# Kernel tuning notes

Hardware: AMD Instinct MI355X
Metric: run time of the kernel (lower is better)

Reference implementation:

```python
import jax, jax.numpy as jnp
import numpy as np

N_NODES = 50000
N_EDGES = 1000000
D_IN = 128
HID = 64
N_GRAPHS = 256
NEG_SLOPE = 0.2


def _gatv2_layer(x, src, dst, Wl, Wr, att, b, n_nodes):
    # lin_l applied to source nodes, lin_r to target nodes (PyG GATv2Conv, heads=1)
    xl = x @ Wl.T  # [N, C]
    xr = x @ Wr.T  # [N, C]
    e = jax.nn.leaky_relu(xl[src] + xr[dst], NEG_SLOPE)  # [E, C]
    logits = e @ att  # [E]
    # segment softmax over destination node
    m = jax.ops.segment_max(logits, dst, num_segments=n_nodes)
    ex = jnp.exp(logits - m[dst])
    den = jax.ops.segment_sum(ex, dst, num_segments=n_nodes)
    alpha = ex / den[dst]  # [E]
    out = jax.ops.segment_sum(alpha[:, None] * xl[src], dst, num_segments=n_nodes)
    return out + b


def setup_inputs() -> dict:
    key = jax.random.key(0)
    ks = jax.random.split(key, 32)
    x = jax.random.normal(ks[0], (N_NODES, D_IN), dtype=jnp.float32)
    edge_index = jax.random.randint(ks[1], (2, N_EDGES), 0, N_NODES, dtype=jnp.int64)
    batch = jnp.sort(jax.random.randint(ks[2], (N_NODES,), 0, N_GRAPHS, dtype=jnp.int64))
    inp = {"x": x, "edge_index": edge_index, "batch": batch}
    dims = [D_IN, HID, HID]  # input dim per layer
    kidx = 3
    for i, din in enumerate(dims):
        inp[f"Wl{i}"] = jax.random.normal(ks[kidx], (HID, din), dtype=jnp.float32) * 0.1; kidx += 1
        inp[f"Wr{i}"] = jax.random.normal(ks[kidx], (HID, din), dtype=jnp.float32) * 0.1; kidx += 1
        inp[f"att{i}"] = jax.random.normal(ks[kidx], (HID,), dtype=jnp.float32) * 0.1; kidx += 1
        inp[f"b{i}"] = jnp.zeros((HID,), dtype=jnp.float32)
        inp[f"Rw{i}"] = jax.random.normal(ks[kidx], (HID, din), dtype=jnp.float32) * 0.1; kidx += 1
        inp[f"Rb{i}"] = jnp.zeros((HID,), dtype=jnp.float32)
    inp["Wf"] = jax.random.normal(ks[kidx], (1, HID), dtype=jnp.float32) * 0.1
    inp["bf"] = jnp.zeros((1,), dtype=jnp.float32)
    return inp


def reference(x, edge_index, batch, Wl0, Wr0, att0, b0, Rw0, Rb0,
              Wl1, Wr1, att1, b1, Rw1, Rb1,
              Wl2, Wr2, att2, b2, Rw2, Rb2, Wf, bf):
    n = x.shape[0]
    # add_self_loops=True (PyG default)
    loops = jnp.arange(n, dtype=edge_index.dtype)
    src = jnp.concatenate([edge_index[0], loops])
    dst = jnp.concatenate([edge_index[1], loops])
    layers = [(Wl0, Wr0, att0, b0, Rw0, Rb0),
              (Wl1, Wr1, att1, b1, Rw1, Rb1),
              (Wl2, Wr2, att2, b2, Rw2, Rb2)]
    for i, (Wl, Wr, att, b, Rw, Rb) in enumerate(layers):
        h = _gatv2_layer(x, src, dst, Wl, Wr, att, b, n) + (x @ Rw.T + Rb)  # res=True
        # norm=None -> Identity; dropout inactive at inference
        x = jax.nn.relu(h) if i < len(layers) - 1 else h
    # global_mean_pool
    sums = jax.ops.segment_sum(x, batch, num_segments=N_GRAPHS)
    cnt = jax.ops.segment_sum(jnp.ones((n,), x.dtype), batch, num_segments=N_GRAPHS)
    pooled = sums / jnp.maximum(cnt, 1.0)[:, None]
    return pooled @ Wf.T + bf
```

## Files before the change

### kernel.cpp

```cpp
#include <hip/hip_runtime.h>


#define NN 50000
#define NE 1000000
#define HID 64
#define DIN0 128
#define NG 256
#define NEG 0.2f

#define SCHUNK 1024
#define SNB ((NN + SCHUNK - 1) / SCHUNK)

typedef float f32x4 __attribute__((ext_vector_type(4)));
typedef short s8v __attribute__((ext_vector_type(8)));
typedef short s4v __attribute__((ext_vector_type(4)));
typedef __bf16 bf16x8 __attribute__((ext_vector_type(8)));
typedef _Float16 h2v __attribute__((ext_vector_type(2)));
typedef unsigned short u16;

__device__ __forceinline__ unsigned short f2bf(float f) {
    unsigned u = __float_as_uint(f);
    u = u + 0x7fffu + ((u >> 16) & 1u);
    return (unsigned short)(u >> 16);
}
__device__ __forceinline__ float bf2f(unsigned short v) {
    return __uint_as_float(((unsigned)v) << 16);
}
__device__ __forceinline__ short split_hi(float x) {
    return (short)f2bf(x);
}
__device__ __forceinline__ short split_lo(float x, short hi) {
    return (short)f2bf(x - bf2f((unsigned short)hi));
}
__device__ __forceinline__ h2v u2h(unsigned u) { return __builtin_bit_cast(h2v, u); }
__device__ __forceinline__ unsigned h2u(h2v h) { return __builtin_bit_cast(unsigned, h); }
__device__ __forceinline__ float hx(unsigned u, int hi) {
    h2v h = __builtin_bit_cast(h2v, u);
    return (float)h[hi];
}

__global__ __launch_bounds__(256) void k_wt_all(
        const float* __restrict__ Wl0, const float* __restrict__ Wr0, const float* __restrict__ Rw0,
        const float* __restrict__ Wl1, const float* __restrict__ Wr1, const float* __restrict__ Rw1,
        const float* __restrict__ Wl2, const float* __restrict__ Wr2, const float* __restrict__ Rw2,
        short* __restrict__ Ws0, short* __restrict__ Ws1, short* __restrict__ Ws2,
        int* __restrict__ startg, int* __restrict__ endg) {
    int i = blockIdx.x * 256 + threadIdx.x;
    if (i < 2 * NG) {
        if (i < NG) startg[i] = 0; else endg[i - NG] = 0;
    }
    const int L0N = 3 * HID * DIN0;
    const int L1N = 3 * HID * HID;
    if (i >= L0N + 2 * L1N) return;
    const float* Wm; short* Ws; int din, local;
    if (i < L0N) {
        local = i; din = DIN0; Ws = Ws0;
        int m = local / (DIN0 * HID);
        Wm = (m == 0) ? Wl0 : (m == 1) ? Wr0 : Rw0;
    } else if (i < L0N + L1N) {
        local = i - L0N; din = HID; Ws = Ws1;
        int m = local / (HID * HID);
        Wm = (m == 0) ? Wl1 : (m == 1) ? Wr1 : Rw1;
    } else {
        local = i - L0N - L1N; din = HID; Ws = Ws2;
        int m = local / (HID * HID);
        Wm = (m == 0) ? Wl2 : (m == 1) ? Wr2 : Rw2;
    }
    int m = local / (din * HID);
    int r = local - m * (din * HID);
    int c = r / din, k = r - c * din;
    float w = Wm[c * din + k];
    short hi = split_hi(w);
    short lo = split_lo(w, hi);
    Ws[(((m * 2 + 0) * HID + c) * din) + k] = hi;
    Ws[(((m * 2 + 1) * HID + c) * din) + k] = lo;
}

__global__ void k_bounds(const int* __restrict__ batch,
                         int* __restrict__ startg, int* __restrict__ endg,
                         int* __restrict__ cnt8) {
    int i = blockIdx.x * 256 + threadIdx.x;
    if (i >= NN) return;
#pragma unroll
    for (int g = 0; g < 8; g++) cnt8[g * NN + i] = 0;
    int g = batch[i];
    if (i == 0 || batch[i - 1] != g) startg[g] = i;
    if (i == NN - 1 || batch[i + 1] != g) endg[g] = i + 1;
}

__global__ __launch_bounds__(256) void k_hist8(const int* __restrict__ edst,
                                               int* __restrict__ cnt8,
                                               u16* __restrict__ rank) {
    int* mycnt = cnt8 + (blockIdx.x & 7) * NN;
    for (int e = blockIdx.x * 256 + threadIdx.x; e < NE; e += 512 * 256) {
        int r = atomicAdd(&mycnt[edst[e]], 1);
        rank[e] = (u16)r;
    }
}

__global__ void k_hist_red(int* __restrict__ cnt8, int* __restrict__ cnt) {
    int i = blockIdx.x * 256 + threadIdx.x;
    if (i >= NN) return;
    int s = 1;
#pragma unroll
    for (int g = 0; g < 8; g++) {
        int t = cnt8[g * NN + i];
        cnt8[g * NN + i] = s;
        s += t;
    }
    cnt[i] = s;
}

__global__ __launch_bounds__(256) void k_scan_part(const int* __restrict__ cnt,
                                                   int* __restrict__ part) {
    __shared__ int ws[4];
    int b = blockIdx.x, t = threadIdx.x;
    int i0 = b * SCHUNK + t * 4;
    int s = 0;
#pragma unroll
    for (int j = 0; j < 4; j++) {
        int i = i0 + j;
        if (i < NN) s += cnt[i];
    }
#pragma unroll
    for (int o = 32; o; o >>= 1) s += __shfl_xor(s, o, 64);
    if ((t & 63) == 0) ws[t >> 6] = s;
    __syncthreads();
    if (t == 0) part[b] = ws[0] + ws[1] + ws[2] + ws[3];
}

__global__ void k_scan_small(const int* __restrict__ part, int* __restrict__ partScan) {
    __shared__ int sh[SNB];
    int t = threadIdx.x;
    if (t < SNB) sh[t] = part[t];
    __syncthreads();
    if (t < SNB) {
        int s = 0;
        for (int i = 0; i < t; i++) s += sh[i];
        partScan[t] = s;
    }
}

__global__ __launch_bounds__(256) void k_scan_emit(const int* __restrict__ cnt,
                                                   const int* __restrict__ partScan,
                                                   int* __restrict__ off,
                                                   u16* __restrict__ srcs) {
    __shared__ int tsum[256];
    int b = blockIdx.x, t = threadIdx.x;
    int i0 = b * SCHUNK + t * 4;
    int e[4], p[4];
    int s = 0;
#pragma unroll
    for (int j = 0; j < 4; j++) {
        int i = i0 + j;
        e[j] = (i < NN) ? cnt[i] : 0;
        p[j] = s;
        s += e[j];
    }
    tsum[t] = s;
    __syncthreads();
    for (int d = 1; d < 256; d <<= 1) {
        int v = (t >= d) ? tsum[t - d] : 0;
        __syncthreads();
        tsum[t] += v;
        __syncthreads();
    }
    int base = partScan[b] + ((t == 0) ? 0 : tsum[t - 1]);
#pragma unroll
    for (int j = 0; j < 4; j++) {
        int i = i0 + j;
        if (i < NN) {
            int v = base + p[j];
            off[i] = v;
            srcs[v] = (u16)i;
            if (i == NN - 1) off[NN] = v + e[j];
        }
    }
}

__global__ __launch_bounds__(256) void k_scatter_rank(
        const int* __restrict__ esrc, const int* __restrict__ edst,
        const int* __restrict__ off, const int* __restrict__ cnt8,
        const u16* __restrict__ rank, u16* __restrict__ srcs) {
    int e = blockIdx.x * 256 + threadIdx.x;
    if (e >= NE) return;
    int d = edst[e];
    int slice = (e >> 8) & 7;
    int pos = off[d] + cnt8[slice * NN + d] + (int)rank[e];
    srcs[pos] = (u16)esrc[e];
}

template <int DIN, bool RELU>
__global__ __launch_bounds__(256, 3) void k_gemm(
        const float* __restrict__ xin, const short* __restrict__ Ws,
        const float* __restrict__ bvec, const float* __restrict__ rb,
        _Float16* __restrict__ xl16, float* __restrict__ xr, float* __restrict__ acc) {
    constexpr int LROW = 40;
    __shared__ short lds[20480];
    short* xhi = lds;
    short* xlo = lds + 2560;

    const int tid = threadIdx.x;
    const int w = tid >> 6;
    const int lane = tid & 63;
    const int col = lane & 15;
    const int quad = lane >> 4;
    const int nb0 = blockIdx.x * 64;

    f32x4 d[3][4];
#pragma unroll
    for (int m = 0; m < 3; m++)
#pragma unroll
        for (int ct = 0; ct < 4; ct++) d[m][ct] = (f32x4){0.f, 0.f, 0.f, 0.f};

    for (int c0 = 0; c0 < DIN; c0 += 32) {
        if (c0) __syncthreads();
        for (int u = tid; u < 512; u += 256) {
            int row = u >> 3, kq = u & 7;
            int n = nb0 + row;
            float4 v = make_float4(0.f, 0.f, 0.f, 0.f);
            if (n < NN) {
                v = *(const float4*)&xin[(size_t)n * DIN + c0 + 4 * kq];
                if (RELU) {
                    v.x = fmaxf(v.x, 0.f); v.y = fmaxf(v.y, 0.f);
                    v.z = fmaxf(v.z, 0.f); v.w = fmaxf(v.w, 0.f);
                }
            }
            s4v h, l;
            short h0 = split_hi(v.x), l0 = split_lo(v.x, h0);
            short h1 = split_hi(v.y), l1 = split_lo(v.y, h1);
            short h2 = split_hi(v.z), l2 = split_lo(v.z, h2);
            short h3 = split_hi(v.w), l3 = split_lo(v.w, h3);
            h[0] = h0; h[1] = h1; h[2] = h2; h[3] = h3;
            l[0] = l0; l[1] = l1; l[2] = l2; l[3] = l3;
            *(s4v*)&xhi[row * LROW + 4 * kq] = h;
            *(s4v*)&xlo[row * LROW + 4 * kq] = l;
        }
        for (int u = tid; u < 1536; u += 256) {
            int mp = u >> 8;
            int r = u & 255;
            int c = r >> 2, q = r & 3;
            s8v v = *(const s8v*)&Ws[((mp * HID + c) * DIN) + c0 + 8 * q];
            *(s8v*)&lds[5120 + mp * 2560 + c * LROW + 8 * q] = v;
        }
        __syncthreads();

        bf16x8 a_h = __builtin_bit_cast(bf16x8,
            *(const s8v*)&xhi[(w * 16 + col) * LROW + quad * 8]);
        bf16x8 a_l = __builtin_bit_cast(bf16x8,
            *(const s8v*)&xlo[(w * 16 + col) * LROW + quad * 8]);

#pragma unroll
        for (int m = 0; m < 3; m++) {
#pragma unroll
            for (int ct = 0; ct < 4; ct++) {
                bf16x8 b_h = __builtin_bit_cast(bf16x8,
                    *(const s8v*)&lds[5120 + (m * 2 + 0) * 2560 + (ct * 16 + col) * LROW + quad * 8]);
                bf16x8 b_l = __builtin_bit_cast(bf16x8,
                    *(const s8v*)&lds[5120 + (m * 2 + 1) * 2560 + (ct * 16 + col) * LROW + quad * 8]);
                d[m][ct] = __builtin_amdgcn_mfma_f32_16x16x32_bf16(a_h, b_h, d[m][ct], 0, 0, 0);
                d[m][ct] = __builtin_amdgcn_mfma_f32_16x16x32_bf16(a_h, b_l, d[m][ct], 0, 0, 0);
                d[m][ct] = __builtin_amdgcn_mfma_f32_16x16x32_bf16(a_l, b_h, d[m][ct], 0, 0, 0);
            }
        }
    }

#pragma unroll
    for (int r = 0; r < 4; r++) {
        int n = nb0 + w * 16 + quad * 4 + r;
        if (n >= NN) continue;
        size_t base = (size_t)n * HID;
#pragma unroll
        for (int ct = 0; ct < 4; ct++) {
            int c = ct * 16 + col;
            xl16[base + c] = (_Float16)d[0][ct][r];
            xr[base + c] = d[1][ct][r];
            acc[base + c] = d[2][ct][r] + bvec[c] + rb[c];
        }
    }
}

__global__ __launch_bounds__(256) void k_attn_dst(
        const int* __restrict__ off, const u16* __restrict__ srcs,
        const _Float16* __restrict__ xl16, const float* __restrict__ xr,
        const float* __restrict__ att, float* __restrict__ acc) {
    const int lane = threadIdx.x & 63;
    const int d = blockIdx.x * 4 + (threadIdx.x >> 6);
    if (d >= NN) return;
    const int e = lane >> 3;
    const int cg = lane & 7;

    const float4* xr4 = (const float4*)&xr[(size_t)d * HID + 8 * cg];
    float4 xra = xr4[0], xrb = xr4[1];
    const float4* at4 = (const float4*)&att[8 * cg];
    float4 ata = at4[0], atb = at4[1];
    h2v xh0 = {(_Float16)xra.x, (_Float16)xra.y};
    h2v xh1 = {(_Float16)xra.z, (_Float16)xra.w};
    h2v xh2 = {(_Float16)xrb.x, (_Float16)xrb.y};
    h2v xh3 = {(_Float16)xrb.z, (_Float16)xrb.w};
    h2v a6h0 = {(_Float16)(0.6f * ata.x), (_Float16)(0.6f * ata.y)};
    h2v a6h1 = {(_Float16)(0.6f * ata.z), (_Float16)(0.6f * ata.w)};
    h2v a6h2 = {(_Float16)(0.6f * atb.x), (_Float16)(0.6f * atb.y)};
    h2v a6h3 = {(_Float16)(0.6f * atb.z), (_Float16)(0.6f * atb.w)};
    h2v a4h0 = {(_Float16)(0.4f * ata.x), (_Float16)(0.4f * ata.y)};
    h2v a4h1 = {(_Float16)(0.4f * ata.z), (_Float16)(0.4f * ata.w)};
    h2v a4h2 = {(_Float16)(0.4f * atb.x), (_Float16)(0.4f * atb.y)};
    h2v a4h3 = {(_Float16)(0.4f * atb.z), (_Float16)(0.4f * atb.w)};

#define EDGE_LOGIT(S, U, T)                                                    \
    {                                                                          \
        U = *(const uint4*)&xl16[(size_t)(S) * HID + 8 * cg];                  \
        h2v _v; unsigned _a; float _ps;                                        \
        _v = u2h(U.x) + xh0; _a = h2u(_v) & 0x7FFF7FFFu;                       \
        _ps = __builtin_amdgcn_fdot2(a6h0, _v, 0.f, false);                    \
        _ps = __builtin_amdgcn_fdot2(a4h0, u2h(_a), _ps, false);               \
        _v = u2h(U.y) + xh1; _a = h2u(_v) & 0x7FFF7FFFu;                       \
        _ps = __builtin_amdgcn_fdot2(a6h1, _v, _ps, false);                    \
        _ps = __builtin_amdgcn_fdot2(a4h1, u2h(_a), _ps, false);               \
        _v = u2h(U.z) + xh2; _a = h2u(_v) & 0x7FFF7FFFu;                       \
        _ps = __builtin_amdgcn_fdot2(a6h2, _v, _ps, false);                    \
        _ps = __builtin_amdgcn_fdot2(a4h2, u2h(_a), _ps, false);               \
        _v = u2h(U.w) + xh3; _a = h2u(_v) & 0x7FFF7FFFu;                       \
        _ps = __builtin_amdgcn_fdot2(a6h3, _v, _ps, false);                    \
        _ps = __builtin_amdgcn_fdot2(a4h3, u2h(_a), _ps, false);               \
        _ps += __shfl_xor(_ps, 1, 64);                                         \
        _ps += __shfl_xor(_ps, 2, 64);                                         \
        _ps += __shfl_xor(_ps, 4, 64);                                         \
        T = _ps;                                                               \
    }

#define ACC8(OP)                                                               \
    oA.x = OP(oA.x, hx(U0.x, 0), hx(U1.x, 0));                                 \
    oA.y = OP(oA.y, hx(U0.x, 1), hx(U1.x, 1));                                 \
    oA.z = OP(oA.z, hx(U0.y, 0), hx(U1.y, 0));                                 \
    oA.w = OP(oA.w, hx(U0.y, 1), hx(U1.y, 1));                                 \
    oB.x = OP(oB.x, hx(U0.z, 0), hx(U1.z, 0));                                 \
    oB.y = OP(oB.y, hx(U0.z, 1), hx(U1.z, 1));                                 \
    oB.z = OP(oB.z, hx(U0.w, 0), hx(U1.w, 0));                                 \
    oB.w = OP(oB.w, hx(U0.w, 1), hx(U1.w, 1));
#define OP_RS(o, x0, x1) fmaf(o, corr, fmaf(p0, x0, p1 * (x1)))
#define OP_NR(o, x0, x1) fmaf(p0, x0, fmaf(p1, (x1), o))

    float m = -INFINITY, l = 0.f;
    float4 oA = make_float4(0.f, 0.f, 0.f, 0.f);
    float4 oB = make_float4(0.f, 0.f, 0.f, 0.f);

    const int lo = off[d], deg = off[d + 1] - lo;
    int sv = 0;
    if (lane < 16) sv = (int)srcs[lo + min(lane, deg - 1)];
    for (int base = 0; base < deg; base += 16) {
        int svc = sv;
        if (base + 16 < deg && lane < 16)
            sv = (int)srcs[lo + min(base + 16 + lane, deg - 1)];
        int s0 = __shfl(svc, e, 64);
        int s1 = __shfl(svc, e + 8, 64);

        uint4 U0, U1; float t0, t1;
        EDGE_LOGIT(s0, U0, t0);
        EDGE_LOGIT(s1, U1, t1);
        if (base + e >= deg) t0 = -INFINITY;
        if (base + 8 + e >= deg) t1 = -INFINITY;

        float cm = fmaxf(t0, t1);
        cm = fmaxf(cm, __shfl_xor(cm, 8, 64));
        cm = fmaxf(cm, __shfl_xor(cm, 16, 64));
        cm = fmaxf(cm, __shfl_xor(cm, 32, 64));
        if (cm > m) {
            float corr = __expf(m - cm);
            float p0 = __expf(t0 - cm);
            float p1 = __expf(t1 - cm);
            m = cm;
            l = fmaf(l, corr, p0 + p1);
            ACC8(OP_RS)
        } else {
            float p0 = __expf(t0 - m);
            float p1 = __expf(t1 - m);
            l += p0 + p1;
            ACC8(OP_NR)
        }
    }
#undef EDGE_LOGIT
#undef ACC8
#undef OP_RS
#undef OP_NR

#pragma unroll
    for (int w = 8; w <= 32; w <<= 1) {
        l    += __shfl_xor(l, w, 64);
        oA.x += __shfl_xor(oA.x, w, 64); oA.y += __shfl_xor(oA.y, w, 64);
        oA.z += __shfl_xor(oA.z, w, 64); oA.w += __shfl_xor(oA.w, w, 64);
        oB.x += __shfl_xor(oB.x, w, 64); oB.y += __shfl_xor(oB.y, w, 64);
        oB.z += __shfl_xor(oB.z, w, 64); oB.w += __shfl_xor(oB.w, w, 64);
    }

    if (e == 0) {
        float inv = 1.f / l;
        float4* a4 = (float4*)&acc[(size_t)d * HID + 8 * cg];
        float4 c0 = a4[0], c1 = a4[1];
        c0.x += oA.x * inv; c0.y += oA.y * inv;
        c0.z += oA.z * inv; c0.w += oA.w * inv;
        c1.x += oB.x * inv; c1.y += oB.y * inv;
        c1.z += oB.z * inv; c1.w += oB.w * inv;
        a4[0] = c0; a4[1] = c1;
    }
}

__global__ __launch_bounds__(512) void k_pool_final(
        const float* __restrict__ acc,
        const int* __restrict__ startg, const int* __restrict__ endg,
        const float* __restrict__ Wf, const float* __restrict__ bf_,
        float* __restrict__ out) {
    __shared__ float red[8][HID];
    const int g = blockIdx.x;
    const int c = threadIdx.x & 63;
    const int j = threadIdx.x >> 6;
    const int s = startg[g], epos = endg[g];

    float sum = 0.f;
    for (int n = s + j; n < epos; n += 8)
        sum += acc[(size_t)n * HID + c];
    red[j][c] = sum;
    __syncthreads();

    if (threadIdx.x < HID) {
        float tot = 0.f;
#pragma unroll
        for (int w = 0; w < 8; w++) tot += red[w][c];
        float cntf = (float)(epos - s);
        float v = tot / fmaxf(cntf, 1.f) * Wf[c];
#pragma unroll
        for (int o = 32; o; o >>= 1) v += __shfl_xor(v, o, 64);
        if (c == 0) out[g] = v + bf_[0];
    }
}

extern "C" void kernel_launch(void* const* d_in, const int* in_sizes, int n_in,
                              void* d_out, int out_size, void* d_ws, size_t ws_size,
                              hipStream_t stream) {
    const float* x   = (const float*)d_in[0];
    const int* eidx  = (const int*)d_in[1];
    const int* batch = (const int*)d_in[2];
    const int* esrc = eidx;
    const int* edst = eidx + NE;
    const float* Wf  = (const float*)d_in[21];
    const float* bfb = (const float*)d_in[22];

    float* wsf = (float*)d_ws;
    const size_t NN64 = (size_t)NN * HID;
    _Float16* xl16 = (_Float16*)wsf;
    float* xr     = wsf + NN64;
    float* acc0   = xr + NN64;
    float* acc1   = acc0 + NN64;
    short* Ws0    = (short*)(acc1 + NN64);
    short* Ws1    = Ws0 + 2 * 3 * HID * DIN0;
    short* Ws2    = Ws1 + 2 * 3 * HID * HID;
    int*   ccnt   = (int*)(Ws2 + 2 * 3 * HID * HID);
    int*   startg = ccnt + NN;
    int*   endg   = startg + NG;
    int*   off    = endg + NG;
    int*   part   = off + NN + 1;
    int*   partSc = part + SNB;
    int*   cnt8   = partSc + SNB;
    u16*   rank   = (u16*)(cnt8 + 8 * NN);
    u16*   srcs   = rank + NE;

    k_wt_all<<<(3 * HID * DIN0 + 2 * 3 * HID * HID + 255) / 256, 256, 0, stream>>>(
        (const float*)d_in[3], (const float*)d_in[4], (const float*)d_in[7],
        (const float*)d_in[9], (const float*)d_in[10], (const float*)d_in[13],
        (const float*)d_in[15], (const float*)d_in[16], (const float*)d_in[19],
        Ws0, Ws1, Ws2, startg, endg);
    k_bounds<<<(NN + 255) / 256, 256, 0, stream>>>(batch, startg, endg, cnt8);

    k_hist8<<<512, 256, 0, stream>>>(edst, cnt8, rank);
    k_hist_red<<<(NN + 255) / 256, 256, 0, stream>>>(cnt8, ccnt);
    k_scan_part<<<SNB, 256, 0, stream>>>(ccnt, part);
    k_scan_small<<<1, 64, 0, stream>>>(part, partSc);
    k_scan_emit<<<SNB, 256, 0, stream>>>(ccnt, partSc, off, srcs);
    k_scatter_rank<<<(NE + 255) / 256, 256, 0, stream>>>(esrc, edst, off, cnt8, rank, srcs);

    const short* Wss[3] = {Ws0, Ws1, Ws2};
    float* accs[4] = {acc0, acc0, acc1, acc0};
    const int gemm_grid = (NN + 63) / 64;
    for (int L = 0; L < 3; L++) {
        const float* att = (const float*)d_in[3 + L * 6 + 2];
        const float* b   = (const float*)d_in[3 + L * 6 + 3];
        const float* Rb  = (const float*)d_in[3 + L * 6 + 5];
        float* accOut = accs[L + 1];

        if (L == 0)
            k_gemm<DIN0, false><<<gemm_grid, 256, 0, stream>>>(
                x, Wss[0], b, Rb, xl16, xr, accOut);
        else
            k_gemm<HID, true><<<gemm_grid, 256, 0, stream>>>(
                accs[L], Wss[L], b, Rb, xl16, xr, accOut);

        k_attn_dst<<<(NN + 3) / 4, 256, 0, stream>>>(off, srcs, xl16, xr, att, accOut);
    }

    k_pool_final<<<NG, 512, 0, stream>>>(accs[3], startg, endg, Wf, bfb, (float*)d_out);
}
```

Before: 358.1 us.

## Process 32 edges per attention iteration with fp16 dot aggregation and fp16 xr

The attention kernel now handles 32 edges per loop iteration (four per lane group) instead of 16, which exposes more independent gathers per wave. The weighted aggregation uses packed fp16 fdot2 with fp16 softmax weights in place of scalar fp32 FMAs, and the online-softmax rescale is split out of the accumulation. xr is stored as fp16 by the GEMM, and the scaled attention vectors are precomputed once in the weight-prep kernel, which cuts per-node conversion and load traffic. The cost is lower precision, since probabilities and xr are rounded to fp16, and higher register pressure from four in-flight edge vectors.

```diff
diff --git a/kernel.cpp b/kernel.cpp
--- a/kernel.cpp
+++ b/kernel.cpp
@@ -34,20 +34,31 @@
 }
 __device__ __forceinline__ h2v u2h(unsigned u) { return __builtin_bit_cast(h2v, u); }
 __device__ __forceinline__ unsigned h2u(h2v h) { return __builtin_bit_cast(unsigned, h); }
-__device__ __forceinline__ float hx(unsigned u, int hi) {
-    h2v h = __builtin_bit_cast(h2v, u);
-    return (float)h[hi];
+__device__ __forceinline__ h2v pklo(unsigned a, unsigned b) {
+    return u2h(__builtin_amdgcn_perm(b, a, 0x05040100u));
+}
+__device__ __forceinline__ h2v pkhi(unsigned a, unsigned b) {
+    return u2h(__builtin_amdgcn_perm(b, a, 0x07060302u));
 }
 
 __global__ __launch_bounds__(256) void k_wt_all(
         const float* __restrict__ Wl0, const float* __restrict__ Wr0, const float* __restrict__ Rw0,
         const float* __restrict__ Wl1, const float* __restrict__ Wr1, const float* __restrict__ Rw1,
         const float* __restrict__ Wl2, const float* __restrict__ Wr2, const float* __restrict__ Rw2,
+        const float* __restrict__ att0, const float* __restrict__ att1, const float* __restrict__ att2,
         short* __restrict__ Ws0, short* __restrict__ Ws1, short* __restrict__ Ws2,
+        _Float16* __restrict__ attp,
         int* __restrict__ startg, int* __restrict__ endg) {
     int i = blockIdx.x * 256 + threadIdx.x;
     if (i < 2 * NG) {
         if (i < NG) startg[i] = 0; else endg[i - NG] = 0;
+    }
+    if (i < 3 * HID) {
+        int L = i >> 6, c = i & 63;
+        const float* at = (L == 0) ? att0 : (L == 1) ? att1 : att2;
+        float a = at[c];
+        attp[L * 2 * HID + c] = (_Float16)(0.6f * a);
+        attp[L * 2 * HID + HID + c] = (_Float16)(0.4f * a);
     }
     const int L0N = 3 * HID * DIN0;
     const int L1N = 3 * HID * HID;
@@ -194,7 +205,7 @@
 __global__ __launch_bounds__(256, 3) void k_gemm(
         const float* __restrict__ xin, const short* __restrict__ Ws,
         const float* __restrict__ bvec, const float* __restrict__ rb,
-        _Float16* __restrict__ xl16, float* __restrict__ xr, float* __restrict__ acc) {
+        _Float16* __restrict__ xl16, _Float16* __restrict__ xr16, float* __restrict__ acc) {
     constexpr int LROW = 40;
     __shared__ short lds[20480];
     short* xhi = lds;
@@ -274,7 +285,7 @@
         for (int ct = 0; ct < 4; ct++) {
             int c = ct * 16 + col;
             xl16[base + c] = (_Float16)d[0][ct][r];
-            xr[base + c] = d[1][ct][r];
+            xr16[base + c] = (_Float16)d[1][ct][r];
             acc[base + c] = d[2][ct][r] + bvec[c] + rb[c];
         }
     }
@@ -282,107 +293,105 @@
 
 __global__ __launch_bounds__(256) void k_attn_dst(
         const int* __restrict__ off, const u16* __restrict__ srcs,
-        const _Float16* __restrict__ xl16, const float* __restrict__ xr,
-        const float* __restrict__ att, float* __restrict__ acc) {
+        const _Float16* __restrict__ xl16, const _Float16* __restrict__ xr16,
+        const _Float16* __restrict__ attL, float* __restrict__ acc) {
     const int lane = threadIdx.x & 63;
     const int d = blockIdx.x * 4 + (threadIdx.x >> 6);
     if (d >= NN) return;
     const int e = lane >> 3;
     const int cg = lane & 7;
 
-    const float4* xr4 = (const float4*)&xr[(size_t)d * HID + 8 * cg];
-    float4 xra = xr4[0], xrb = xr4[1];
-    const float4* at4 = (const float4*)&att[8 * cg];
-    float4 ata = at4[0], atb = at4[1];
-    h2v xh0 = {(_Float16)xra.x, (_Float16)xra.y};
-    h2v xh1 = {(_Float16)xra.z, (_Float16)xra.w};
-    h2v xh2 = {(_Float16)xrb.x, (_Float16)xrb.y};
-    h2v xh3 = {(_Float16)xrb.z, (_Float16)xrb.w};
-    h2v a6h0 = {(_Float16)(0.6f * ata.x), (_Float16)(0.6f * ata.y)};
-    h2v a6h1 = {(_Float16)(0.6f * ata.z), (_Float16)(0.6f * ata.w)};
-    h2v a6h2 = {(_Float16)(0.6f * atb.x), (_Float16)(0.6f * atb.y)};
-    h2v a6h3 = {(_Float16)(0.6f * atb.z), (_Float16)(0.6f * atb.w)};
-    h2v a4h0 = {(_Float16)(0.4f * ata.x), (_Float16)(0.4f * ata.y)};
-    h2v a4h1 = {(_Float16)(0.4f * ata.z), (_Float16)(0.4f * ata.w)};
-    h2v a4h2 = {(_Float16)(0.4f * atb.x), (_Float16)(0.4f * atb.y)};
-    h2v a4h3 = {(_Float16)(0.4f * atb.z), (_Float16)(0.4f * atb.w)};
+    uint4 X = *(const uint4*)&xr16[(size_t)d * HID + 8 * cg];
+    uint4 A6 = *(const uint4*)&attL[8 * cg];
+    uint4 A4 = *(const uint4*)&attL[HID + 8 * cg];
+    h2v xh0 = u2h(X.x), xh1 = u2h(X.y), xh2 = u2h(X.z), xh3 = u2h(X.w);
+    h2v a60 = u2h(A6.x), a61 = u2h(A6.y), a62 = u2h(A6.z), a63 = u2h(A6.w);
+    h2v a40 = u2h(A4.x), a41 = u2h(A4.y), a42 = u2h(A4.z), a43 = u2h(A4.w);
 
 #define EDGE_LOGIT(S, U, T)                                                    \
     {                                                                          \
         U = *(const uint4*)&xl16[(size_t)(S) * HID + 8 * cg];                  \
         h2v _v; unsigned _a; float _ps;                                        \
         _v = u2h(U.x) + xh0; _a = h2u(_v) & 0x7FFF7FFFu;                       \
-        _ps = __builtin_amdgcn_fdot2(a6h0, _v, 0.f, false);                    \
-        _ps = __builtin_amdgcn_fdot2(a4h0, u2h(_a), _ps, false);               \
+        _ps = __builtin_amdgcn_fdot2(a60, _v, 0.f, false);                     \
+        _ps = __builtin_amdgcn_fdot2(a40, u2h(_a), _ps, false);                \
         _v = u2h(U.y) + xh1; _a = h2u(_v) & 0x7FFF7FFFu;                       \
-        _ps = __builtin_amdgcn_fdot2(a6h1, _v, _ps, false);                    \
-        _ps = __builtin_amdgcn_fdot2(a4h1, u2h(_a), _ps, false);               \
+        _ps = __builtin_amdgcn_fdot2(a61, _v, _ps, false);                     \
+        _ps = __builtin_amdgcn_fdot2(a41, u2h(_a), _ps, false);                \
         _v = u2h(U.z) + xh2; _a = h2u(_v) & 0x7FFF7FFFu;                       \
-        _ps = __builtin_amdgcn_fdot2(a6h2, _v, _ps, false);                    \
-        _ps = __builtin_amdgcn_fdot2(a4h2, u2h(_a), _ps, false);               \
+        _ps = __builtin_amdgcn_fdot2(a62, _v, _ps, false);                     \
+        _ps = __builtin_amdgcn_fdot2(a42, u2h(_a), _ps, false);                \
         _v = u2h(U.w) + xh3; _a = h2u(_v) & 0x7FFF7FFFu;                       \
-        _ps = __builtin_amdgcn_fdot2(a6h3, _v, _ps, false);                    \
-        _ps = __builtin_amdgcn_fdot2(a4h3, u2h(_a), _ps, false);               \
+        _ps = __builtin_amdgcn_fdot2(a63, _v, _ps, false);                     \
+        _ps = __builtin_amdgcn_fdot2(a43, u2h(_a), _ps, false);                \
         _ps += __shfl_xor(_ps, 1, 64);                                         \
         _ps += __shfl_xor(_ps, 2, 64);                                         \
         _ps += __shfl_xor(_ps, 4, 64);                                         \
         T = _ps;                                                               \
     }
 
-#define ACC8(OP)                                                               \
-    oA.x = OP(oA.x, hx(U0.x, 0), hx(U1.x, 0));                                 \
-    oA.y = OP(oA.y, hx(U0.x, 1), hx(U1.x, 1));                                 \
-    oA.z = OP(oA.z, hx(U0.y, 0), hx(U1.y, 0));                                 \
-    oA.w = OP(oA.w, hx(U0.y, 1), hx(U1.y, 1));                                 \
-    oB.x = OP(oB.x, hx(U0.z, 0), hx(U1.z, 0));                                 \
-    oB.y = OP(oB.y, hx(U0.z, 1), hx(U1.z, 1));                                 \
-    oB.z = OP(oB.z, hx(U0.w, 0), hx(U1.w, 0));                                 \
-    oB.w = OP(oB.w, hx(U0.w, 1), hx(U1.w, 1));
-#define OP_RS(o, x0, x1) fmaf(o, corr, fmaf(p0, x0, p1 * (x1)))
-#define OP_NR(o, x0, x1) fmaf(p0, x0, fmaf(p1, (x1), o))
-
     float m = -INFINITY, l = 0.f;
     float4 oA = make_float4(0.f, 0.f, 0.f, 0.f);
     float4 oB = make_float4(0.f, 0.f, 0.f, 0.f);
 
     const int lo = off[d], deg = off[d + 1] - lo;
     int sv = 0;
-    if (lane < 16) sv = (int)srcs[lo + min(lane, deg - 1)];
-    for (int base = 0; base < deg; base += 16) {
+    if (lane < 32) sv = (int)srcs[lo + min(lane, deg - 1)];
+    for (int base = 0; base < deg; base += 32) {
         int svc = sv;
-        if (base + 16 < deg && lane < 16)
-            sv = (int)srcs[lo + min(base + 16 + lane, deg - 1)];
+        if (base + 32 < deg && lane < 32)
+            sv = (int)srcs[lo + min(base + 32 + lane, deg - 1)];
         int s0 = __shfl(svc, e, 64);
         int s1 = __shfl(svc, e + 8, 64);
-
-        uint4 U0, U1; float t0, t1;
+        int s2 = __shfl(svc, e + 16, 64);
+        int s3 = __shfl(svc, e + 24, 64);
+
+        uint4 U0, U1, U2, U3; float t0, t1, t2, t3;
         EDGE_LOGIT(s0, U0, t0);
         EDGE_LOGIT(s1, U1, t1);
+        EDGE_LOGIT(s2, U2, t2);
+        EDGE_LOGIT(s3, U3, t3);
         if (base + e >= deg) t0 = -INFINITY;
         if (base + 8 + e >= deg) t1 = -INFINITY;
-
-        float cm = fmaxf(t0, t1);
+        if (base + 16 + e >= deg) t2 = -INFINITY;
+        if (base + 24 + e >= deg) t3 = -INFINITY;
+
+        float cm = fmaxf(fmaxf(t0, t1), fmaxf(t2, t3));
         cm = fmaxf(cm, __shfl_xor(cm, 8, 64));
         cm = fmaxf(cm, __shfl_xor(cm, 16, 64));
         cm = fmaxf(cm, __shfl_xor(cm, 32, 64));
         if (cm > m) {
             float corr = __expf(m - cm);
-            float p0 = __expf(t0 - cm);
-            float p1 = __expf(t1 - cm);
             m = cm;
-            l = fmaf(l, corr, p0 + p1);
-            ACC8(OP_RS)
-        } else {
-            float p0 = __expf(t0 - m);
-            float p1 = __expf(t1 - m);
-            l += p0 + p1;
-            ACC8(OP_NR)
+            l *= corr;
+            oA.x *= corr; oA.y *= corr; oA.z *= corr; oA.w *= corr;
+            oB.x *= corr; oB.y *= corr; oB.z *= corr; oB.w *= corr;
         }
+        float p0 = __expf(t0 - m);
+        float p1 = __expf(t1 - m);
+        float p2 = __expf(t2 - m);
+        float p3 = __expf(t3 - m);
+        l += (p0 + p1) + (p2 + p3);
+        h2v p01 = {(_Float16)p0, (_Float16)p1};
+        h2v p23 = {(_Float16)p2, (_Float16)p3};
+        oA.x = __builtin_amdgcn_fdot2(p01, pklo(U0.x, U1.x), oA.x, false);
+        oA.x = __builtin_amdgcn_fdot2(p23, pklo(U2.x, U3.x), oA.x, false);
+        oA.y = __builtin_amdgcn_fdot2(p01, pkhi(U0.x, U1.x), oA.y, false);
+        oA.y = __builtin_amdgcn_fdot2(p23, pkhi(U2.x, U3.x), oA.y, false);
+        oA.z = __builtin_amdgcn_fdot2(p01, pklo(U0.y, U1.y), oA.z, false);
+        oA.z = __builtin_amdgcn_fdot2(p23, pklo(U2.y, U3.y), oA.z, false);
+        oA.w = __builtin_amdgcn_fdot2(p01, pkhi(U0.y, U1.y), oA.w, false);
+        oA.w = __builtin_amdgcn_fdot2(p23, pkhi(U2.y, U3.y), oA.w, false);
+        oB.x = __builtin_amdgcn_fdot2(p01, pklo(U0.z, U1.z), oB.x, false);
+        oB.x = __builtin_amdgcn_fdot2(p23, pklo(U2.z, U3.z), oB.x, false);
+        oB.y = __builtin_amdgcn_fdot2(p01, pkhi(U0.z, U1.z), oB.y, false);
+        oB.y = __builtin_amdgcn_fdot2(p23, pkhi(U2.z, U3.z), oB.y, false);
+        oB.z = __builtin_amdgcn_fdot2(p01, pklo(U0.w, U1.w), oB.z, false);
+        oB.z = __builtin_amdgcn_fdot2(p23, pklo(U2.w, U3.w), oB.z, false);
+        oB.w = __builtin_amdgcn_fdot2(p01, pkhi(U0.w, U1.w), oB.w, false);
+        oB.w = __builtin_amdgcn_fdot2(p23, pkhi(U2.w, U3.w), oB.w, false);
     }
 #undef EDGE_LOGIT
-#undef ACC8
-#undef OP_RS
-#undef OP_NR
 
 #pragma unroll
     for (int w = 8; w <= 32; w <<= 1) {
@@ -448,8 +457,8 @@
     float* wsf = (float*)d_ws;
     const size_t NN64 = (size_t)NN * HID;
     _Float16* xl16 = (_Float16*)wsf;
-    float* xr     = wsf + NN64;
-    float* acc0   = xr + NN64;
+    _Float16* xr16 = (_Float16*)(wsf + NN64);
+    float* acc0   = wsf + 2 * NN64;
     float* acc1   = acc0 + NN64;
     short* Ws0    = (short*)(acc1 + NN64);
     short* Ws1    = Ws0 + 2 * 3 * HID * DIN0;
@@ -463,12 +472,14 @@
     int*   cnt8   = partSc + SNB;
     u16*   rank   = (u16*)(cnt8 + 8 * NN);
     u16*   srcs   = rank + NE;
+    _Float16* attp = (_Float16*)(srcs + NE + NN);
 
     k_wt_all<<<(3 * HID * DIN0 + 2 * 3 * HID * HID + 255) / 256, 256, 0, stream>>>(
         (const float*)d_in[3], (const float*)d_in[4], (const float*)d_in[7],
         (const float*)d_in[9], (const float*)d_in[10], (const float*)d_in[13],
         (const float*)d_in[15], (const float*)d_in[16], (const float*)d_in[19],
-        Ws0, Ws1, Ws2, startg, endg);
+        (const float*)d_in[5], (const float*)d_in[11], (const float*)d_in[17],
+        Ws0, Ws1, Ws2, attp, startg, endg);
     k_bounds<<<(NN + 255) / 256, 256, 0, stream>>>(batch, startg, endg, cnt8);
 
     k_hist8<<<512, 256, 0, stream>>>(edst, cnt8, rank);
@@ -482,19 +493,19 @@
     float* accs[4] = {acc0, acc0, acc1, acc0};
     const int gemm_grid = (NN + 63) / 64;
     for (int L = 0; L < 3; L++) {
-        const float* att = (const float*)d_in[3 + L * 6 + 2];
         const float* b   = (const float*)d_in[3 + L * 6 + 3];
         const float* Rb  = (const float*)d_in[3 + L * 6 + 5];
         float* accOut = accs[L + 1];
 
         if (L == 0)
             k_gemm<DIN0, false><<<gemm_grid, 256, 0, stream>>>(
-                x, Wss[0], b, Rb, xl16, xr, accOut);
+                x, Wss[0], b, Rb, xl16, xr16, accOut);
         else
             k_gemm<HID, true><<<gemm_grid, 256, 0, stream>>>(
-                accs[L], Wss[L], b, Rb, xl16, xr, accOut);
-
-        k_attn_dst<<<(NN + 3) / 4, 256, 0, stream>>>(off, srcs, xl16, xr, att, accOut);
+                accs[L], Wss[L], b, Rb, xl16, xr16, accOut);
+
+        k_attn_dst<<<(NN + 3) / 4, 256, 0, stream>>>(
+            off, srcs, xl16, xr16, attp + L * 2 * HID, accOut);
     }
 
     k_pool_final<<<NG, 512, 0, stream>>>(accs[3], startg, endg, Wf, bfb, (float*)d_out);
```

Result: faster. 347.7 us (-2.9%).
